# Optimization experiments

Measured on AMD Instinct MI355X. Metric: run time of the kernel, lower is better.

## Reference

```python
import jax, jax.numpy as jnp
import numpy as np
import math

FILTER_SIZE = 11
FILTER_SIGMA = 1.5
C1 = 0.01 ** 2
C2 = 0.03 ** 2
PAD = FILTER_SIZE // 2


def _make_gauss_kernel(sigma, kernel_size, channel=3):
    mean = np.floor(0.5 * kernel_size)
    x = np.arange(kernel_size, dtype=np.float64)
    k1d = np.exp(-((x - mean) ** 2) / (2 * sigma ** 2)) * (1.0 / (2 * math.pi * sigma ** 2))
    k2d = np.outer(k1d, k1d).astype(np.float32)
    k2d = k2d / k2d.sum()
    # OIHW depthwise kernel: [channel, 1, k, k]
    return np.broadcast_to(k2d[None, None], (channel, 1, kernel_size, kernel_size)).copy()


def _depthwise_blur(x, kernel):
    # x: [B, 3, H, W], kernel: [3, 1, k, k]; groups=3, SAME padding (k//2)
    return jax.lax.conv_general_dilated(
        x, kernel,
        window_strides=(1, 1),
        padding=[(PAD, PAD), (PAD, PAD)],
        dimension_numbers=('NCHW', 'OIHW', 'NCHW'),
        feature_group_count=3,
    )


def setup_inputs() -> dict:
    key = jax.random.key(0)
    k1, k2 = jax.random.split(key)
    B, C, H, W = 32, 3, 512, 512
    image1 = jax.random.uniform(k1, (B, C, H, W), dtype=jnp.float32)
    image2 = jax.random.uniform(k2, (B, C, H, W), dtype=jnp.float32)
    gauss_kernel = jnp.asarray(_make_gauss_kernel(FILTER_SIGMA, FILTER_SIZE, channel=3))
    return {"image1": image1, "image2": image2, "gauss_kernel": gauss_kernel}


def reference(image1, image2, gauss_kernel):
    mu1 = _depthwise_blur(image1, gauss_kernel)
    mu2 = _depthwise_blur(image2, gauss_kernel)
    mu1_sq = mu1 * mu1
    mu2_sq = mu2 * mu2
    mu1_mu2 = mu1 * mu2
    sig1_sq = _depthwise_blur(image1 * image1, gauss_kernel) - mu1_sq
    sig2_sq = _depthwise_blur(image2 * image2, gauss_kernel) - mu2_sq
    sig1_sig2 = _depthwise_blur(image1 * image2, gauss_kernel) - mu1_mu2
    ssim_num = (2.0 * mu1_mu2 + C1) * (2.0 * sig1_sig2 + C2)
    ssim_den = (mu1_sq + mu2_sq + C1) * (sig1_sq + sig2_sq + C2)
    ssim_map = ssim_num / ssim_den
    dssim_map = (1.0 - ssim_map) * 0.5
    return dssim_map.mean()  # size_average=True
```

## Files before the change

### kernel.cpp

```cpp
#include <hip/hip_runtime.h>
#include <math.h>


namespace {
constexpr int IMG = 512;
constexpr int TW = 32;
constexpr int RB = 64;
constexpr int RING = RB + 10;
constexpr int SLOT = 44;
constexpr int XGN = TW / 8;
constexpr int NCHUNK = IMG / RB;
constexpr int CTILES = IMG / TW;
constexpr int NIMG = 96;
constexpr float C1c = 1e-4f;
constexpr float C2c = 9e-4f;
constexpr float INV_N = 1.0f / 25165824.0f;
}

__global__ void dssim_zero(float* ws) { ws[0] = 0.0f; }

__global__ void dssim_final(const float* __restrict__ ws, float* __restrict__ out) {
  out[0] = ws[0] * INV_N;
}

__global__ __launch_bounds__(256, 3) void dssim_main(
    const float* __restrict__ im1, const float* __restrict__ im2,
    const float* __restrict__ gk, float* __restrict__ ws)
{
  __shared__ float sR[XGN * RING * SLOT];

  const int tid = threadIdx.x;
  const int bid = blockIdx.x;
  const int img = bid >> 4;
  const int tsx = bid & 15;
  const int X0s = tsx * TW;

  const float* __restrict__ p1 = im1 + (size_t)img * (IMG * IMG);
  const float* __restrict__ p2 = im2 + (size_t)img * (IMG * IMG);

  float wt[11];
  {
    float ic = 1.0f / sqrtf(gk[5 * 11 + 5]);
    #pragma unroll
    for (int i = 0; i < 11; ++i) wt[i] = gk[i * 11 + 5] * ic;
  }

  const int c   = tid & 31;
  const int yg  = tid >> 5;
  const int xg3 = c >> 3;
  const int cl  = c & 7;

  float lsum = 0.f;

  for (int k = 0; k < NCHUNK; ++k) {
    const int r0    = (k == 0) ? -5 : RB * k + 5;
    const int ntask = (k == 0) ? XGN * RING : XGN * RB;
    for (int t = tid; t < ntask; t += 256) {
      const int xg = t & 3, dr = t >> 2;
      const int r  = r0 + dr;
      const int rr = (r + 5) % RING;
      const int X0 = X0s + xg * 8;
      const int cb = X0 - 8;

      float a24[24], b24[24];
      if ((unsigned)r < (unsigned)IMG) {
        const float* row1 = p1 + r * IMG;
        const float* row2 = p2 + r * IMG;
        if (cb >= 0 && cb + 24 <= IMG) {
          #pragma unroll
          for (int i = 0; i < 6; ++i) {
            float4 v1 = *(const float4*)(row1 + cb + 4 * i);
            float4 v2 = *(const float4*)(row2 + cb + 4 * i);
            a24[4*i+0] = v1.x; a24[4*i+1] = v1.y; a24[4*i+2] = v1.z; a24[4*i+3] = v1.w;
            b24[4*i+0] = v2.x; b24[4*i+1] = v2.y; b24[4*i+2] = v2.z; b24[4*i+3] = v2.w;
          }
        } else {
          #pragma unroll
          for (int e = 0; e < 24; ++e) {
            int cc = cb + e;
            bool ok = (unsigned)cc < (unsigned)IMG;
            a24[e] = ok ? row1[cc] : 0.f;
            b24[e] = ok ? row2[cc] : 0.f;
          }
        }
      } else {
        #pragma unroll
        for (int e = 0; e < 24; ++e) { a24[e] = 0.f; b24[e] = 0.f; }
      }

      float o0[8], o1[8], o2[8], o3[8], o4[8];
      #pragma unroll
      for (int j = 0; j < 8; ++j) { o0[j]=0.f; o1[j]=0.f; o2[j]=0.f; o3[j]=0.f; o4[j]=0.f; }
      #pragma unroll
      for (int e = 0; e < 18; ++e) {
        float va = a24[e + 3], vb = b24[e + 3];
        float pa = va * va, pb = vb * vb, pab = va * vb;
        #pragma unroll
        for (int j = 0; j < 8; ++j) {
          int kk = e - j;
          if (kk >= 0 && kk < 11) {
            float w = wt[kk];
            o0[j] = fmaf(w, va,  o0[j]);
            o1[j] = fmaf(w, vb,  o1[j]);
            o2[j] = fmaf(w, pa,  o2[j]);
            o3[j] = fmaf(w, pb,  o3[j]);
            o4[j] = fmaf(w, pab, o4[j]);
          }
        }
      }

      const int base = (xg * RING + rr) * SLOT;
      #pragma unroll
      for (int j = 0; j < 8; ++j)
        *(float4*)&sR[base + 4 * j] = make_float4(o0[j], o1[j], o2[j], o3[j]);
      *(float4*)&sR[base + 32] = make_float4(o4[0], o4[1], o4[2], o4[3]);
      *(float4*)&sR[base + 36] = make_float4(o4[4], o4[5], o4[6], o4[7]);
    }
    __syncthreads();

    float mu1[8], mu2[8], e11[8], e22[8], e12[8];
    #pragma unroll
    for (int j = 0; j < 8; ++j) { mu1[j]=0.f; mu2[j]=0.f; e11[j]=0.f; e22[j]=0.f; e12[j]=0.f; }

    const int rbase = (RB * k + yg * 8) % RING;
    #pragma unroll
    for (int rrr = 0; rrr < 18; ++rrr) {
      int idx = rbase + rrr;
      if (idx >= RING) idx -= RING;
      const int a = (xg3 * RING + idx) * SLOT;
      float4 v4 = *(const float4*)&sR[a + 4 * cl];
      float  v5 = sR[a + 32 + cl];
      #pragma unroll
      for (int j = 0; j < 8; ++j) {
        int kk = rrr - j;
        if (kk >= 0 && kk < 11) {
          float w = wt[kk];
          mu1[j] = fmaf(w, v4.x, mu1[j]);
          mu2[j] = fmaf(w, v4.y, mu2[j]);
          e11[j] = fmaf(w, v4.z, e11[j]);
          e22[j] = fmaf(w, v4.w, e22[j]);
          e12[j] = fmaf(w, v5,  e12[j]);
        }
      }
    }

    #pragma unroll
    for (int j = 0; j < 8; ++j) {
      float m1 = mu1[j], m2 = mu2[j];
      float m1s = m1 * m1, m2s = m2 * m2, m12 = m1 * m2;
      float s11 = e11[j] - m1s, s22 = e22[j] - m2s, s12 = e12[j] - m12;
      float num = (2.f * m12 + C1c) * (2.f * s12 + C2c);
      float den = (m1s + m2s + C1c) * (s11 + s22 + C2c);
      lsum += (1.f - num / den) * 0.5f;
    }
    __syncthreads();
  }

  #pragma unroll
  for (int off = 32; off > 0; off >>= 1) lsum += __shfl_down(lsum, off);
  if ((tid & 63) == 0) atomicAdd(ws, lsum);
}

extern "C" void kernel_launch(void* const* d_in, const int* in_sizes, int n_in,
                              void* d_out, int out_size, void* d_ws, size_t ws_size,
                              hipStream_t stream) {
  const float* im1 = (const float*)d_in[0];
  const float* im2 = (const float*)d_in[1];
  const float* gk  = (const float*)d_in[2];
  float* out = (float*)d_out;
  float* ws  = (float*)d_ws;

  hipLaunchKernelGGL(dssim_zero, dim3(1), dim3(1), 0, stream, ws);
  hipLaunchKernelGGL(dssim_main, dim3(NIMG * CTILES), dim3(256), 0, stream,
                     im1, im2, gk, ws);
  hipLaunchKernelGGL(dssim_final, dim3(1), dim3(1), 0, stream, ws, out);
}
```

Baseline: 302.9 us.

## Software-prefetch next chunk's rows into registers and use fast reciprocal

Restructures the chunk loop so each thread issues global loads for the next chunk's input rows before the vertical pass and SSIM computation of the current chunk. The prefetched rows are then run through the horizontal blur into the LDS ring after a barrier. This aims to hide global memory latency behind compute. It also replaces the division with a hardware reciprocal approximation. The costs are 48 extra live registers per thread, which could cut occupancy under launch_bounds(256,3), and a slight loss of precision.

```diff
diff --git a/kernel.cpp b/kernel.cpp
--- a/kernel.cpp
+++ b/kernel.cpp
@@ -45,79 +45,96 @@
     for (int i = 0; i < 11; ++i) wt[i] = gk[i * 11 + 5] * ic;
   }
 
+  const int xg = tid & 3;
+  const int dr = tid >> 2;
+  const int cbf = X0s + xg * 8 - 8;
+  const bool intf = (cbf >= 0) && (cbf + 24 <= IMG);
+
   const int c   = tid & 31;
   const int yg  = tid >> 5;
   const int xg3 = c >> 3;
   const int cl  = c & 7;
 
+  auto loadrow = [&](const float* __restrict__ p, int r, int cbx, bool inter,
+                     float4* dst) {
+    const float* row = p + r * IMG;
+    if (inter) {
+      #pragma unroll
+      for (int i = 0; i < 6; ++i) dst[i] = *(const float4*)(row + cbx + 4 * i);
+    } else {
+      #pragma unroll
+      for (int i = 0; i < 6; ++i) {
+        int c0 = cbx + 4 * i;
+        float e0 = ((unsigned)(c0 + 0) < (unsigned)IMG) ? row[c0 + 0] : 0.f;
+        float e1 = ((unsigned)(c0 + 1) < (unsigned)IMG) ? row[c0 + 1] : 0.f;
+        float e2 = ((unsigned)(c0 + 2) < (unsigned)IMG) ? row[c0 + 2] : 0.f;
+        float e3 = ((unsigned)(c0 + 3) < (unsigned)IMG) ? row[c0 + 3] : 0.f;
+        dst[i] = make_float4(e0, e1, e2, e3);
+      }
+    }
+  };
+
+  auto hcompute = [&](const float4* A, const float4* B, bool valid,
+                      int xgw, int ringrow) {
+    float a24[24], b24[24];
+    #pragma unroll
+    for (int i = 0; i < 6; ++i) {
+      a24[4*i+0] = valid ? A[i].x : 0.f;  a24[4*i+1] = valid ? A[i].y : 0.f;
+      a24[4*i+2] = valid ? A[i].z : 0.f;  a24[4*i+3] = valid ? A[i].w : 0.f;
+      b24[4*i+0] = valid ? B[i].x : 0.f;  b24[4*i+1] = valid ? B[i].y : 0.f;
+      b24[4*i+2] = valid ? B[i].z : 0.f;  b24[4*i+3] = valid ? B[i].w : 0.f;
+    }
+    float o0[8], o1[8], o2[8], o3[8], o4[8];
+    #pragma unroll
+    for (int j = 0; j < 8; ++j) { o0[j]=0.f; o1[j]=0.f; o2[j]=0.f; o3[j]=0.f; o4[j]=0.f; }
+    #pragma unroll
+    for (int e = 0; e < 18; ++e) {
+      float va = a24[e + 3], vb = b24[e + 3];
+      float pa = va * va, pb = vb * vb, pab = va * vb;
+      #pragma unroll
+      for (int j = 0; j < 8; ++j) {
+        int kk = e - j;
+        if (kk >= 0 && kk < 11) {
+          float w = wt[kk];
+          o0[j] = fmaf(w, va,  o0[j]);
+          o1[j] = fmaf(w, vb,  o1[j]);
+          o2[j] = fmaf(w, pa,  o2[j]);
+          o3[j] = fmaf(w, pb,  o3[j]);
+          o4[j] = fmaf(w, pab, o4[j]);
+        }
+      }
+    }
+    const int base = (xgw * RING + ringrow) * SLOT;
+    #pragma unroll
+    for (int j = 0; j < 8; ++j)
+      *(float4*)&sR[base + 4 * j] = make_float4(o0[j], o1[j], o2[j], o3[j]);
+    *(float4*)&sR[base + 32] = make_float4(o4[0], o4[1], o4[2], o4[3]);
+    *(float4*)&sR[base + 36] = make_float4(o4[4], o4[5], o4[6], o4[7]);
+  };
+
+  for (int t = tid; t < XGN * RING; t += 256) {
+    int sxg = t & 3, sdr = t >> 2;
+    int r = sdr - 5;
+    int scb = X0s + sxg * 8 - 8;
+    bool sint = (scb >= 0) && (scb + 24 <= IMG);
+    float4 LA[6], LB[6];
+    bool valid = (unsigned)r < (unsigned)IMG;
+    if (valid) { loadrow(p1, r, scb, sint, LA); loadrow(p2, r, scb, sint, LB); }
+    hcompute(LA, LB, valid, sxg, r + 5);
+  }
+
+  float4 A[6], B[6];
+  {
+    int r = RB + 5 + dr;
+    if ((unsigned)r < (unsigned)IMG) {
+      loadrow(p1, r, cbf, intf, A);
+      loadrow(p2, r, cbf, intf, B);
+    }
+  }
+  __syncthreads();
+
   float lsum = 0.f;
-
   for (int k = 0; k < NCHUNK; ++k) {
-    const int r0    = (k == 0) ? -5 : RB * k + 5;
-    const int ntask = (k == 0) ? XGN * RING : XGN * RB;
-    for (int t = tid; t < ntask; t += 256) {
-      const int xg = t & 3, dr = t >> 2;
-      const int r  = r0 + dr;
-      const int rr = (r + 5) % RING;
-      const int X0 = X0s + xg * 8;
-      const int cb = X0 - 8;
-
-      float a24[24], b24[24];
-      if ((unsigned)r < (unsigned)IMG) {
-        const float* row1 = p1 + r * IMG;
-        const float* row2 = p2 + r * IMG;
-        if (cb >= 0 && cb + 24 <= IMG) {
-          #pragma unroll
-          for (int i = 0; i < 6; ++i) {
-            float4 v1 = *(const float4*)(row1 + cb + 4 * i);
-            float4 v2 = *(const float4*)(row2 + cb + 4 * i);
-            a24[4*i+0] = v1.x; a24[4*i+1] = v1.y; a24[4*i+2] = v1.z; a24[4*i+3] = v1.w;
-            b24[4*i+0] = v2.x; b24[4*i+1] = v2.y; b24[4*i+2] = v2.z; b24[4*i+3] = v2.w;
-          }
-        } else {
-          #pragma unroll
-          for (int e = 0; e < 24; ++e) {
-            int cc = cb + e;
-            bool ok = (unsigned)cc < (unsigned)IMG;
-            a24[e] = ok ? row1[cc] : 0.f;
-            b24[e] = ok ? row2[cc] : 0.f;
-          }
-        }
-      } else {
-        #pragma unroll
-        for (int e = 0; e < 24; ++e) { a24[e] = 0.f; b24[e] = 0.f; }
-      }
-
-      float o0[8], o1[8], o2[8], o3[8], o4[8];
-      #pragma unroll
-      for (int j = 0; j < 8; ++j) { o0[j]=0.f; o1[j]=0.f; o2[j]=0.f; o3[j]=0.f; o4[j]=0.f; }
-      #pragma unroll
-      for (int e = 0; e < 18; ++e) {
-        float va = a24[e + 3], vb = b24[e + 3];
-        float pa = va * va, pb = vb * vb, pab = va * vb;
-        #pragma unroll
-        for (int j = 0; j < 8; ++j) {
-          int kk = e - j;
-          if (kk >= 0 && kk < 11) {
-            float w = wt[kk];
-            o0[j] = fmaf(w, va,  o0[j]);
-            o1[j] = fmaf(w, vb,  o1[j]);
-            o2[j] = fmaf(w, pa,  o2[j]);
-            o3[j] = fmaf(w, pb,  o3[j]);
-            o4[j] = fmaf(w, pab, o4[j]);
-          }
-        }
-      }
-
-      const int base = (xg * RING + rr) * SLOT;
-      #pragma unroll
-      for (int j = 0; j < 8; ++j)
-        *(float4*)&sR[base + 4 * j] = make_float4(o0[j], o1[j], o2[j], o3[j]);
-      *(float4*)&sR[base + 32] = make_float4(o4[0], o4[1], o4[2], o4[3]);
-      *(float4*)&sR[base + 36] = make_float4(o4[4], o4[5], o4[6], o4[7]);
-    }
-    __syncthreads();
-
     float mu1[8], mu2[8], e11[8], e22[8], e12[8];
     #pragma unroll
     for (int j = 0; j < 8; ++j) { mu1[j]=0.f; mu2[j]=0.f; e11[j]=0.f; e22[j]=0.f; e12[j]=0.f; }
@@ -151,9 +168,23 @@
       float s11 = e11[j] - m1s, s22 = e22[j] - m2s, s12 = e12[j] - m12;
       float num = (2.f * m12 + C1c) * (2.f * s12 + C2c);
       float den = (m1s + m2s + C1c) * (s11 + s22 + C2c);
-      lsum += (1.f - num / den) * 0.5f;
+      lsum += (1.f - num * __builtin_amdgcn_rcpf(den)) * 0.5f;
     }
     __syncthreads();
+
+    if (k < NCHUNK - 1) {
+      int r = RB * (k + 1) + 5 + dr;
+      bool valid = (unsigned)r < (unsigned)IMG;
+      hcompute(A, B, valid, xg, (r + 5) % RING);
+      if (k < NCHUNK - 2) {
+        int rn = RB * (k + 2) + 5 + dr;
+        if ((unsigned)rn < (unsigned)IMG) {
+          loadrow(p1, rn, cbf, intf, A);
+          loadrow(p2, rn, cbf, intf, B);
+        }
+      }
+      __syncthreads();
+    }
   }
 
   #pragma unroll
```

New measurement: 712.3 us. 135% more time.
